# Optimization experiments

Measured on AMD Instinct MI355X. Metric: run time of the kernel, lower is better.

The kernel has to match this reference:

```python
import jax, jax.numpy as jnp
import numpy as np

VOCAB, HID, L, HEADS, INTER, MAXSEQ, NCLS = 30522, 128, 2, 2, 512, 512, 2
HEAD = HID // HEADS
B, S = 128, 512


def _tlin(x, W, b):
    # TernaryLinear: threshold-quantize W to {-1,0,1} with per-tensor scale,
    # then ordinary linear. delta = 0.7*mean|W|, alpha = mean|W| over kept entries.
    absW = jnp.abs(W)
    delta = 0.7 * jnp.mean(absW)
    mask = (absW > delta).astype(W.dtype)
    alpha = jnp.sum(absW * mask) / jnp.maximum(jnp.sum(mask), 1.0)
    Wq = jnp.sign(W) * mask * alpha  # [out, in]
    return jnp.einsum('...i,oi->...o', x, Wq) + b


def _ln(x, g, b, eps=1e-5):
    m = jnp.mean(x, axis=-1, keepdims=True)
    v = jnp.var(x, axis=-1, keepdims=True)
    return (x - m) * jax.lax.rsqrt(v + eps) * g + b


def setup_inputs() -> dict:
    key = jax.random.key(0)
    ks = iter(jax.random.split(key, 64))
    n = lambda shape, s=0.02: jax.random.normal(next(ks), shape, dtype=jnp.float32) * s
    inp = {
        'input_ids': jax.random.randint(next(ks), (B, S), 0, VOCAB, dtype=jnp.int32).astype(jnp.int64),
        'tok_emb': n((VOCAB, HID)),
        'pos_emb': n((MAXSEQ, HID)),
        'ln_g': jnp.ones((HID,), jnp.float32), 'ln_b': jnp.zeros((HID,), jnp.float32),
        'qw': n((L, HID, HID)), 'qb': jnp.zeros((L, HID), jnp.float32),
        'kw': n((L, HID, HID)), 'kb': jnp.zeros((L, HID), jnp.float32),
        'vw': n((L, HID, HID)), 'vb': jnp.zeros((L, HID), jnp.float32),
        'aow': n((L, HID, HID)), 'aob': jnp.zeros((L, HID), jnp.float32),
        'iw': n((L, INTER, HID)), 'ib': jnp.zeros((L, INTER), jnp.float32),
        'fow': n((L, HID, INTER)), 'fob': jnp.zeros((L, HID), jnp.float32),
        'ln1g': jnp.ones((L, HID), jnp.float32), 'ln1b': jnp.zeros((L, HID), jnp.float32),
        'ln2g': jnp.ones((L, HID), jnp.float32), 'ln2b': jnp.zeros((L, HID), jnp.float32),
        'clf_w': n((NCLS, HID)), 'clf_b': jnp.zeros((NCLS,), jnp.float32),
    }
    return inp


def reference(input_ids, tok_emb, pos_emb, ln_g, ln_b, qw, qb, kw, kb, vw, vb,
              aow, aob, iw, ib, fow, fob, ln1g, ln1b, ln2g, ln2b, clf_w, clf_b):
    b, s = input_ids.shape
    x = tok_emb[input_ids] + pos_emb[jnp.arange(s)][None, :, :]  # [B,S,H]
    x = _ln(x, ln_g, ln_b)
    scale = 1.0 / (HEAD ** 0.5)
    for l in range(L):
        q = _tlin(x, qw[l], qb[l]).reshape(b, s, HEADS, HEAD)
        k = _tlin(x, kw[l], kb[l]).reshape(b, s, HEADS, HEAD)
        v = _tlin(x, vw[l], vb[l]).reshape(b, s, HEADS, HEAD)
        scores = jnp.einsum('bqhd,bkhd->bhqk', q, k) * scale
        attn = jax.nn.softmax(scores, axis=-1)
        ctx = jnp.einsum('bhqk,bkhd->bqhd', attn, v).reshape(b, s, HID)
        attn_out = _tlin(ctx, aow[l], aob[l])
        x = _ln(x + attn_out, ln1g[l], ln1b[l])
        ff = _tlin(jax.nn.relu(_tlin(x, iw[l], ib[l])), fow[l], fob[l])
        x = _ln(x + ff, ln2g[l], ln2b[l])
    cls = x[:, 0, :]
    logits = _tlin(cls, clf_w, clf_b)  # [B, NCLS]
    return logits
```

## Files before the change

kernel.cpp:

```cpp
#include <hip/hip_runtime.h>

typedef short bf8s __attribute__((ext_vector_type(8)));
typedef float f32x4 __attribute__((ext_vector_type(4)));

#define MFMA16(a, b, c) __builtin_amdgcn_mfma_f32_16x16x32_bf16(a, b, c, 0, 0, 0)

constexpr int S_ = 512, HID_ = 128, B_ = 128, M_ = B_ * S_;

__device__ inline short f2bf(float f) {
  unsigned u = __float_as_uint(f);
  u = (u + 0x7fffu + ((u >> 16) & 1u)) >> 16;
  return (short)u;
}
__device__ inline float bf2f(short s) {
  return __uint_as_float(((unsigned)(unsigned short)s) << 16);
}

__device__ __forceinline__ void async16(void* lds, const void* g) {
  __builtin_amdgcn_global_load_lds(
      (const __attribute__((address_space(1))) unsigned int*)g,
      (__attribute__((address_space(3))) unsigned int*)lds, 16, 0, 0);
}

__device__ __forceinline__ bf8s ldsb(const short* base, int byteoff) {
  return *(const bf8s*)((const char*)base + byteoff);
}

__device__ inline float block_red1024(float v, float* red) {
  #pragma unroll
  for (int m = 32; m >= 1; m >>= 1) v += __shfl_xor(v, m);
  __syncthreads();
  if ((threadIdx.x & 63) == 0) red[threadIdx.x >> 6] = v;
  __syncthreads();
  float t = 0.f;
  #pragma unroll
  for (int i = 0; i < 16; ++i) t += red[i];
  return t;
}

__device__ inline void mat_info(int mat, const float* qw, const float* kw,
                                const float* vw, const float* aow, const float* iw,
                                const float* fw, const float* cw,
                                const float** src, int* n, int* doff, int* lc) {
  if (mat < 6) {
    int l = mat / 3, which = mat % 3;
    const float* t[3] = {qw, kw, vw};
    *src = t[which] + l * 16384; *n = 16384; *doff = l * 49152 + which * 16384;
    *lc = 7;
  } else if (mat < 8) {
    int l = mat - 6;
    *src = aow + l * 16384; *n = 16384; *doff = 98304 + l * 16384; *lc = 7;
  } else if (mat < 10) {
    *src = iw + (mat - 8) * 65536; *n = 65536; *doff = 131072 + (mat - 8) * 65536;
    *lc = 7;
  } else if (mat < 12) {
    *src = fw + (mat - 10) * 65536; *n = 65536; *doff = 262144 + (mat - 10) * 65536;
    *lc = 9;
  } else {
    *src = cw; *n = 256; *doff = 393216; *lc = 0;
  }
}

__global__ __launch_bounds__(1024) void k_qe(const float* qw, const float* kw,
    const float* vw, const float* aow, const float* iw, const float* fw,
    const float* cw, short* WQ,
    const int* __restrict__ ids, const float* __restrict__ tok,
    const float* __restrict__ pos, const float* __restrict__ g,
    const float* __restrict__ bb, short* xb) {
  __shared__ float red[16];
  int tid = threadIdx.x;
  if (blockIdx.x < 13) {
    const float* src; int n, doff, lc;
    mat_info(blockIdx.x, qw, kw, vw, aow, iw, fw, cw, &src, &n, &doff, &lc);
    float s = 0.f;
    for (int i = tid; i < n; i += 1024) s += fabsf(src[i]);
    s = block_red1024(s, red);
    float delta = 0.7f * s / (float)n;
    float s2 = 0.f, c2 = 0.f;
    for (int i = tid; i < n; i += 1024) {
      float a = fabsf(src[i]);
      if (a > delta) { s2 += a; c2 += 1.f; }
    }
    s2 = block_red1024(s2, red);
    c2 = block_red1024(c2, red);
    float alpha = s2 / fmaxf(c2, 1.f);
    if (lc) {
      int nf8 = n >> 3;
      for (int fo8 = tid; fo8 < nf8; fo8 += 1024) {
        int fo = fo8 << 3;
        int tile = fo >> (lc + 4);
        int rem = fo & ((16 << lc) - 1);
        int kblk = rem >> 9;
        int rem2 = rem & 511;
        int sub = rem2 >> 7;
        int r16 = (rem2 >> 3) & 15;
        int r = (tile << 4) | r16;
        int cbase = (kblk << 5) | (sub << 3);
        const float* sp = src + ((size_t)r << lc) + cbase;
        float4 w0 = *(const float4*)(sp);
        float4 w1 = *(const float4*)(sp + 4);
        float wv[8] = {w0.x, w0.y, w0.z, w0.w, w1.x, w1.y, w1.z, w1.w};
        bf8s q;
        #pragma unroll
        for (int j = 0; j < 8; ++j) {
          float w = wv[j];
          q[j] = (fabsf(w) > delta) ? f2bf(w > 0.f ? alpha : -alpha) : (short)0;
        }
        *(bf8s*)(WQ + doff + fo) = q;
      }
    } else {
      for (int i = tid; i < n; i += 1024) {
        float w = src[i];
        WQ[doff + i] = (fabsf(w) > delta) ? f2bf(w > 0.f ? alpha : -alpha) : (short)0;
      }
    }
  } else {
    int wave = tid >> 6, lane = tid & 63;
    int half = lane >> 5, l32 = lane & 31;
    int t = (blockIdx.x - 13) * 32 + wave * 2 + half;
    int s = t & (S_ - 1);
    int id = ids[t];
    int d0 = l32 * 4;
    float4 te = *(const float4*)(tok + (size_t)id * HID_ + d0);
    float4 pe = *(const float4*)(pos + (size_t)s * HID_ + d0);
    float e0 = te.x + pe.x, e1 = te.y + pe.y, e2 = te.z + pe.z, e3 = te.w + pe.w;
    float sum = e0 + e1 + e2 + e3;
    float ssq = e0 * e0 + e1 * e1 + e2 * e2 + e3 * e3;
    #pragma unroll
    for (int m = 16; m >= 1; m >>= 1) {
      sum += __shfl_xor(sum, m);
      ssq += __shfl_xor(ssq, m);
    }
    float mean = sum / 128.f;
    float var = ssq / 128.f - mean * mean;
    float rs = rsqrtf(var + 1e-5f);
    float4 g4 = *(const float4*)(g + d0);
    float4 b4 = *(const float4*)(bb + d0);
    short4 o;
    o.x = f2bf((e0 - mean) * rs * g4.x + b4.x);
    o.y = f2bf((e1 - mean) * rs * g4.y + b4.y);
    o.z = f2bf((e2 - mean) * rs * g4.z + b4.z);
    o.w = f2bf((e3 - mean) * rs * g4.w + b4.w);
    *(short4*)(xb + (size_t)t * HID_ + d0) = o;
  }
}

__global__ __launch_bounds__(256) void k_qkv(
    const short* __restrict__ A, const short* __restrict__ W,
    const float* __restrict__ b0, const float* __restrict__ b1,
    const float* __restrict__ b2, short* outb) {
  __shared__ short Wl[16384];
  int tid = threadIdx.x, lane = tid & 63, wave = tid >> 6;
  int row16 = lane & 15, quad = lane >> 4;
  int tok0 = blockIdx.x * 64 + wave * 16;

  const char* Wm = (const char*)W + blockIdx.y * 32768;
  #pragma unroll
  for (int t = 0; t < 8; ++t)
    async16((char*)Wl + t * 4096 + wave * 1024,
            Wm + t * 4096 + wave * 1024 + lane * 16);

  const short* arow = A + (size_t)(tok0 + row16) * 128 + quad * 8;
  bf8s av[4];
  #pragma unroll
  for (int ki = 0; ki < 4; ++ki) av[ki] = *(const bf8s*)(arow + ki * 32);
  __syncthreads();

  f32x4 acc[8] = {};
  #pragma unroll
  for (int ki = 0; ki < 4; ++ki)
    #pragma unroll
    for (int ot = 0; ot < 8; ++ot) {
      bf8s b = ldsb(Wl, ot * 4096 + ki * 1024 + lane * 16);
      acc[ot] = MFMA16(av[ki], b, acc[ot]);
    }

  const float* bp = (blockIdx.y == 0) ? b0 : ((blockIdx.y == 1) ? b1 : b2);
  float osc = (blockIdx.y == 0) ? 0.125f : 1.0f;
  int m0 = tok0 + quad * 4;
  #pragma unroll
  for (int ot = 0; ot < 8; ++ot) {
    int col = ot * 16 + row16;
    float bi = bp[col];
    #pragma unroll
    for (int r = 0; r < 4; ++r) {
      float v = (acc[ot][r] + bi) * osc;
      outb[(size_t)(m0 + r) * 384 + blockIdx.y * 128 + col] = f2bf(v);
    }
  }
}

template <int DOQKV>
__global__ __launch_bounds__(512, 4) void k_aoff(
    const short* __restrict__ cb, const short* __restrict__ Wa,
    const float* __restrict__ aob, const float* __restrict__ ln1g,
    const float* __restrict__ ln1b, const short* __restrict__ Wi,
    const short* __restrict__ Wf, const float* __restrict__ ib,
    const float* __restrict__ fb, const float* __restrict__ ln2g,
    const float* __restrict__ ln2b, short* xb,
    const short* __restrict__ Wqkv2, const float* __restrict__ qb2,
    const float* __restrict__ kb2, const float* __restrict__ vb2,
    short* qkvout) {
  __shared__ short SM[39936];
  int tid = threadIdx.x, lane = tid & 63, wave = tid >> 6;
  int row16 = lane & 15, quad = lane >> 4;
  int tok0 = blockIdx.x * 128 + wave * 16;
  short* mySt = SM + 16384 + wave * 640;
  short* myX  = SM + 21504 + wave * 2304;
  int xr = lane >> 2, xs = (lane & 3) * 32;
  int lb = lane * 16;

  {
    #pragma unroll
    for (int t = 0; t < 4; ++t)
      async16((char*)SM + t * 8192 + wave * 1024,
              (const char*)Wa + t * 8192 + wave * 1024 + lb);
    const short* src = xb + (size_t)(tok0 + xr) * HID_ + xs;
    bf8s x0 = *(const bf8s*)(src);
    bf8s x1 = *(const bf8s*)(src + 8);
    bf8s x2 = *(const bf8s*)(src + 16);
    bf8s x3 = *(const bf8s*)(src + 24);
    short* dst = myX + xr * 144 + xs;
    *(bf8s*)(dst) = x0;      *(bf8s*)(dst + 8) = x1;
    *(bf8s*)(dst + 16) = x2; *(bf8s*)(dst + 24) = x3;
  }

  const short* arow = cb + (size_t)(tok0 + row16) * 128 + quad * 8;
  bf8s av[4];
  #pragma unroll
  for (int ki = 0; ki < 4; ++ki) av[ki] = *(const bf8s*)(arow + ki * 32);
  __syncthreads();

  f32x4 acc[8] = {};
  #pragma unroll
  for (int ki = 0; ki < 4; ++ki)
    #pragma unroll
    for (int ot = 0; ot < 8; ++ot) {
      bf8s b = ldsb(SM, ot * 4096 + ki * 1024 + lb);
      acc[ot] = MFMA16(av[ki], b, acc[ot]);
    }
  __syncthreads();

  {
    async16((char*)SM + wave * 1024, (const char*)Wi + wave * 1024 + lb);
    async16((char*)SM + 16384 + wave * 1024,
            (const char*)Wf + wave * 16384 + lb);
  }

  {
    float sum[4] = {}, ssq[4] = {};
    #pragma unroll
    for (int ot = 0; ot < 8; ++ot) {
      int col = ot * 16 + row16;
      float bi = aob[col];
      #pragma unroll
      for (int r = 0; r < 4; ++r) {
        float v = acc[ot][r] + bi + bf2f(myX[(quad * 4 + r) * 144 + col]);
        acc[ot][r] = v;
        sum[r] += v; ssq[r] += v * v;
      }
    }
    #pragma unroll
    for (int m = 1; m <= 8; m <<= 1)
      #pragma unroll
      for (int r = 0; r < 4; ++r) {
        sum[r] += __shfl_xor(sum[r], m);
        ssq[r] += __shfl_xor(ssq[r], m);
      }
    float mean[4], rstd[4];
    #pragma unroll
    for (int r = 0; r < 4; ++r) {
      mean[r] = sum[r] / 128.f;
      float var = ssq[r] / 128.f - mean[r] * mean[r];
      rstd[r] = rsqrtf(var + 1e-5f);
    }
    #pragma unroll
    for (int ot = 0; ot < 8; ++ot) {
      int col = ot * 16 + row16;
      float gg = ln1g[col], bb2 = ln1b[col];
      #pragma unroll
      for (int r = 0; r < 4; ++r)
        acc[ot][r] = (acc[ot][r] - mean[r]) * rstd[r] * gg + bb2;
    }
  }

  #pragma unroll
  for (int ot = 0; ot < 8; ++ot) {
    int col = ot * 16 + row16;
    #pragma unroll
    for (int r = 0; r < 4; ++r)
      myX[(quad * 4 + r) * 144 + col] = f2bf(acc[ot][r]);
  }
  #pragma unroll
  for (int ki = 0; ki < 4; ++ki)
    av[ki] = *(const bf8s*)(myX + row16 * 144 + ki * 32 + quad * 8);
  __syncthreads();

  f32x4 acc2[8] = {};
  for (int c = 0; c < 16; ++c) {
    int side = c & 1;
    if (c < 15) {
      int cn = c + 1, sn = cn & 1;
      async16((char*)SM + sn * 8192 + wave * 1024,
              (const char*)Wi + cn * 8192 + wave * 1024 + lb);
      async16((char*)SM + 16384 + sn * 8192 + wave * 1024,
              (const char*)Wf + wave * 16384 + cn * 1024 + lb);
    } else if (DOQKV) {
      async16((char*)SM + wave * 1024, (const char*)Wqkv2 + wave * 1024 + lb);
      async16((char*)SM + 16384 + wave * 1024,
              (const char*)Wqkv2 + 8192 + wave * 1024 + lb);
    }

    #pragma unroll
    for (int ot = 0; ot < 2; ++ot) {
      f32x4 hacc = {};
      #pragma unroll
      for (int ki = 0; ki < 4; ++ki) {
        bf8s b = ldsb(SM, side * 8192 + ot * 4096 + ki * 1024 + lb);
        hacc = MFMA16(av[ki], b, hacc);
      }
      float bi = ib[c * 32 + ot * 16 + row16];
      #pragma unroll
      for (int r = 0; r < 4; ++r)
        mySt[(quad * 4 + r) * 40 + ot * 16 + row16] =
            f2bf(fmaxf(hacc[r] + bi, 0.f));
    }
    bf8s ha = *(const bf8s*)(mySt + row16 * 40 + quad * 8);
    #pragma unroll
    for (int ot = 0; ot < 8; ++ot) {
      bf8s bB = ldsb(SM, 16384 + side * 8192 + ot * 1024 + lb);
      acc2[ot] = MFMA16(ha, bB, acc2[ot]);
    }
    __syncthreads();
  }

  {
    float sum[4] = {}, ssq[4] = {};
    #pragma unroll
    for (int ot = 0; ot < 8; ++ot) {
      int col = ot * 16 + row16;
      float bi = fb[col];
      #pragma unroll
      for (int r = 0; r < 4; ++r) {
        float v = acc2[ot][r] + bi + bf2f(myX[(quad * 4 + r) * 144 + col]);
        acc2[ot][r] = v;
        sum[r] += v; ssq[r] += v * v;
      }
    }
    #pragma unroll
    for (int m = 1; m <= 8; m <<= 1)
      #pragma unroll
      for (int r = 0; r < 4; ++r) {
        sum[r] += __shfl_xor(sum[r], m);
        ssq[r] += __shfl_xor(ssq[r], m);
      }
    float mean[4], rstd[4];
    #pragma unroll
    for (int r = 0; r < 4; ++r) {
      mean[r] = sum[r] / 128.f;
      float var = ssq[r] / 128.f - mean[r] * mean[r];
      rstd[r] = rsqrtf(var + 1e-5f);
    }
    #pragma unroll
    for (int ot = 0; ot < 8; ++ot) {
      int col = ot * 16 + row16;
      float gg = ln2g[col], bb2 = ln2b[col];
      #pragma unroll
      for (int r = 0; r < 4; ++r)
        acc2[ot][r] = (acc2[ot][r] - mean[r]) * rstd[r] * gg + bb2;
    }
  }

  #pragma unroll
  for (int ot = 0; ot < 8; ++ot) {
    int col = ot * 16 + row16;
    #pragma unroll
    for (int r = 0; r < 4; ++r)
      myX[(quad * 4 + r) * 144 + col] = f2bf(acc2[ot][r]);
  }
  {
    const short* src = myX + xr * 144 + xs;
    short* dst = xb + (size_t)(tok0 + xr) * HID_ + xs;
    #pragma unroll
    for (int j = 0; j < 4; ++j)
      *(bf8s*)(dst + j * 8) = *(const bf8s*)(src + j * 8);
  }

  if (DOQKV) {
    bf8s av2[4];
    #pragma unroll
    for (int ki = 0; ki < 4; ++ki)
      av2[ki] = *(const bf8s*)(myX + row16 * 144 + ki * 32 + quad * 8);
    for (int j = 0; j < 6; ++j) {
      int side = j & 1;
      if (j < 5) {
        int jn = j + 1, sn = jn & 1;
        async16((char*)SM + sn * 8192 + wave * 1024,
                (const char*)Wqkv2 + jn * 16384 + wave * 1024 + lb);
        async16((char*)SM + 16384 + sn * 8192 + wave * 1024,
                (const char*)Wqkv2 + jn * 16384 + 8192 + wave * 1024 + lb);
      }
      f32x4 acc3[4] = {};
      #pragma unroll
      for (int ki = 0; ki < 4; ++ki)
        #pragma unroll
        for (int ot = 0; ot < 4; ++ot) {
          int bb_ = (ot < 2) ? side * 8192 + ot * 4096
                             : 16384 + side * 8192 + (ot - 2) * 4096;
          bf8s b = ldsb(SM, bb_ + ki * 1024 + lb);
          acc3[ot] = MFMA16(av2[ki], b, acc3[ot]);
        }
      const float* bp = (j < 2) ? qb2 : ((j < 4) ? kb2 : vb2);
      float osc = (j < 2) ? 0.125f : 1.0f;
      #pragma unroll
      for (int ot = 0; ot < 4; ++ot) {
        int col = ot * 16 + row16;
        float bi = bp[(j & 1) * 64 + col];
        #pragma unroll
        for (int r = 0; r < 4; ++r)
          myX[(quad * 4 + r) * 144 + col] = f2bf((acc3[ot][r] + bi) * osc);
      }
      {
        int xr2 = lane >> 2, xs2 = (lane & 3) * 16;
        const short* src = myX + xr2 * 144 + xs2;
        short* dst = qkvout + (size_t)(tok0 + xr2) * 384 + j * 64 + xs2;
        *(bf8s*)(dst) = *(const bf8s*)(src);
        *(bf8s*)(dst + 8) = *(const bf8s*)(src + 8);
      }
      __syncthreads();
    }
  }
}

__global__ __launch_bounds__(512) void k_attn(const short* __restrict__ qkv,
                                              short* __restrict__ O) {
  __shared__ short Kl[64 * 72];
  __shared__ short Vtl[64 * 72];
  __shared__ short Pl[8][16 * 72];

  int tid = threadIdx.x, lane = tid & 63, wave = tid >> 6;
  int row16 = lane & 15, quad = lane >> 4;
  int b = blockIdx.x >> 2, h = (blockIdx.x >> 1) & 1, qhalf = blockIdx.x & 1;
  const short* base  = qkv + (size_t)b * S_ * 384;
  const short* kbase = base + 128 + h * 64;
  const short* vbase = base + 256 + h * 64;
  int q0 = qhalf * 256 + wave * 32;

  bf8s qa[2][2];
  #pragma unroll
  for (int qf = 0; qf < 2; ++qf) {
    const short* qrow = base + h * 64 +
        (size_t)(q0 + qf * 16 + row16) * 384 + quad * 8;
    qa[qf][0] = *(const bf8s*)(qrow);
    qa[qf][1] = *(const bf8s*)(qrow + 32);
  }

  int krow = tid >> 3, dgk = tid & 7;
  int vkey = tid & 63, dgv = tid >> 6;
  const short* kptr = kbase + (size_t)krow * 384 + dgk * 8;
  const short* vptr = vbase + (size_t)vkey * 384 + dgv * 8;
  bf8s kst = *(const bf8s*)(kptr);
  bf8s vst = *(const bf8s*)(vptr);

  float li[2][4] = {};
  f32x4 oacc[2][4] = {};
  short* myP = &Pl[wave][0];

  for (int kt0 = 0; kt0 < S_; kt0 += 64) {
    if (kt0) __syncthreads();
    *(bf8s*)(&Kl[krow * 72 + dgk * 8]) = kst;
    #pragma unroll
    for (int j = 0; j < 8; ++j) Vtl[(dgv * 8 + j) * 72 + vkey] = vst[j];
    __syncthreads();
    if (kt0 + 64 < S_) {
      kst = *(const bf8s*)(kptr + (size_t)(kt0 + 64) * 384);
      vst = *(const bf8s*)(vptr + (size_t)(kt0 + 64) * 384);
    }

    f32x4 sc[2][4] = {};
    #pragma unroll
    for (int ks = 0; ks < 4; ++ks) {
      const short* kp = &Kl[(ks * 16 + row16) * 72 + quad * 8];
      bf8s k0 = *(const bf8s*)(kp);
      bf8s k1 = *(const bf8s*)(kp + 32);
      sc[0][ks] = MFMA16(qa[0][0], k0, sc[0][ks]);
      sc[0][ks] = MFMA16(qa[0][1], k1, sc[0][ks]);
      sc[1][ks] = MFMA16(qa[1][0], k0, sc[1][ks]);
      sc[1][ks] = MFMA16(qa[1][1], k1, sc[1][ks]);
    }

    #pragma unroll
    for (int qf = 0; qf < 2; ++qf) {
      #pragma unroll
      for (int ks = 0; ks < 4; ++ks)
        #pragma unroll
        for (int r = 0; r < 4; ++r) {
          float pv = __expf(sc[qf][ks][r]);
          li[qf][r] += pv;
          myP[(quad * 4 + r) * 72 + ks * 16 + row16] = f2bf(pv);
        }
      bf8s pa0 = *(const bf8s*)(&myP[row16 * 72 + quad * 8]);
      bf8s pa1 = *(const bf8s*)(&myP[row16 * 72 + 32 + quad * 8]);
      #pragma unroll
      for (int dt = 0; dt < 4; ++dt) {
        const short* vp = &Vtl[(dt * 16 + row16) * 72 + quad * 8];
        bf8s v0 = *(const bf8s*)(vp);
        bf8s v1 = *(const bf8s*)(vp + 32);
        oacc[qf][dt] = MFMA16(pa0, v0, oacc[qf][dt]);
        oacc[qf][dt] = MFMA16(pa1, v1, oacc[qf][dt]);
      }
    }
  }

  #pragma unroll
  for (int qf = 0; qf < 2; ++qf) {
    float inv[4];
    #pragma unroll
    for (int r = 0; r < 4; ++r) {
      float t = li[qf][r];
      #pragma unroll
      for (int m = 1; m <= 8; m <<= 1) t += __shfl_xor(t, m);
      inv[r] = 1.f / t;
    }
    size_t trow = (size_t)(b * S_ + q0 + qf * 16 + quad * 4);
    #pragma unroll
    for (int dt = 0; dt < 4; ++dt)
      #pragma unroll
      for (int r = 0; r < 4; ++r)
        O[(trow + r) * HID_ + h * 64 + dt * 16 + row16] =
            f2bf(oacc[qf][dt][r] * inv[r]);
  }
}

__global__ __launch_bounds__(256) void k_clf(const short* __restrict__ xb,
    const short* __restrict__ Wc, const float* __restrict__ cbias, float* out) {
  int i = threadIdx.x;
  int b = i >> 1, c = i & 1;
  float s = 0.f;
  for (int k = 0; k < HID_; ++k)
    s += bf2f(xb[(size_t)b * S_ * HID_ + k]) * bf2f(Wc[c * HID_ + k]);
  out[b * 2 + c] = s + cbias[c];
}

extern "C" void kernel_launch(void* const* d_in, const int* in_sizes, int n_in,
                              void* d_out, int out_size, void* d_ws, size_t ws_size,
                              hipStream_t stream) {
  const int*   ids     = (const int*)d_in[0];
  const float* tok_emb = (const float*)d_in[1];
  const float* pos_emb = (const float*)d_in[2];
  const float* ln_g    = (const float*)d_in[3];
  const float* ln_bb   = (const float*)d_in[4];
  const float* qw      = (const float*)d_in[5];
  const float* qbias   = (const float*)d_in[6];
  const float* kw      = (const float*)d_in[7];
  const float* kbias   = (const float*)d_in[8];
  const float* vw      = (const float*)d_in[9];
  const float* vbias   = (const float*)d_in[10];
  const float* aow     = (const float*)d_in[11];
  const float* aobias  = (const float*)d_in[12];
  const float* iw      = (const float*)d_in[13];
  const float* ibias   = (const float*)d_in[14];
  const float* fow     = (const float*)d_in[15];
  const float* fbias   = (const float*)d_in[16];
  const float* ln1g    = (const float*)d_in[17];
  const float* ln1b    = (const float*)d_in[18];
  const float* ln2g    = (const float*)d_in[19];
  const float* ln2b    = (const float*)d_in[20];
  const float* clfw    = (const float*)d_in[21];
  const float* clfb    = (const float*)d_in[22];

  char* ws = (char*)d_ws;
  short* WQ  = (short*)ws;
  short* xb  = (short*)(ws + 1048576);
  short* qkv = (short*)(ws + 1048576 + 16777216);
  short* cb_ = qkv + (size_t)M_ * 384;

  k_qe<<<13 + M_ / 32, 1024, 0, stream>>>(qw, kw, vw, aow, iw, fow, clfw, WQ,
                                          ids, tok_emb, pos_emb, ln_g, ln_bb, xb);

  const short* Wqkv0 = WQ;
  const short* Wqkv1 = WQ + 49152;
  const short* Wa0   = WQ + 98304;
  const short* Wa1   = WQ + 98304 + 16384;
  const short* Wi0   = WQ + 131072;
  const short* Wi1   = WQ + 131072 + 65536;
  const short* Wf0   = WQ + 262144;
  const short* Wf1   = WQ + 262144 + 65536;

  k_qkv<<<dim3(M_ / 64, 3), 256, 0, stream>>>(
      xb, Wqkv0, qbias, kbias, vbias, qkv);
  k_attn<<<512, 512, 0, stream>>>(qkv, cb_);
  k_aoff<1><<<M_ / 128, 512, 0, stream>>>(
      cb_, Wa0, aobias, ln1g, ln1b, Wi0, Wf0, ibias, fbias, ln2g, ln2b, xb,
      Wqkv1, qbias + HID_, kbias + HID_, vbias + HID_, qkv);
  k_attn<<<512, 512, 0, stream>>>(qkv, cb_);
  k_aoff<0><<<M_ / 128, 512, 0, stream>>>(
      cb_, Wa1, aobias + HID_, ln1g + HID_, ln1b + HID_, Wi1, Wf1,
      ibias + 512, fbias + HID_, ln2g + HID_, ln2b + HID_, xb,
      nullptr, nullptr, nullptr, nullptr, nullptr);

  k_clf<<<1, 256, 0, stream>>>(xb, WQ + 393216, clfb, (float*)d_out);
}
```

Measured before the change: 306.5 us.

## Unroll weight-stat loads, stage QKV output through LDS, parallelize classifier

Three changes. The ternary-quantization statistics loops now issue eight independent loads per thread per iteration, giving more memory-level parallelism. The QKV projection writes its bf16 results into an LDS scratch tile, reusing the weight buffer after a barrier, and then stores full 16-byte row segments instead of scattered 2-byte writes. The classifier becomes one 64-lane block per batch row with a shuffle reduction instead of a single 256-thread block doing serial dot products. The cost is an extra barrier and LDS round-trip in the QKV kernel.

```diff
diff --git a/kernel.cpp b/kernel.cpp
--- a/kernel.cpp
+++ b/kernel.cpp
@@ -73,13 +73,37 @@
     const float* src; int n, doff, lc;
     mat_info(blockIdx.x, qw, kw, vw, aow, iw, fw, cw, &src, &n, &doff, &lc);
     float s = 0.f;
-    for (int i = tid; i < n; i += 1024) s += fabsf(src[i]);
+    if (n >= 8192) {
+      for (int i0 = tid; i0 < n; i0 += 8192) {
+        float v[8];
+        #pragma unroll
+        for (int j = 0; j < 8; ++j) v[j] = src[i0 + j * 1024];
+        #pragma unroll
+        for (int j = 0; j < 8; ++j) s += fabsf(v[j]);
+      }
+    } else {
+      for (int i = tid; i < n; i += 1024) s += fabsf(src[i]);
+    }
     s = block_red1024(s, red);
     float delta = 0.7f * s / (float)n;
     float s2 = 0.f, c2 = 0.f;
-    for (int i = tid; i < n; i += 1024) {
-      float a = fabsf(src[i]);
-      if (a > delta) { s2 += a; c2 += 1.f; }
+    if (n >= 8192) {
+      for (int i0 = tid; i0 < n; i0 += 8192) {
+        float v[8];
+        #pragma unroll
+        for (int j = 0; j < 8; ++j) v[j] = src[i0 + j * 1024];
+        #pragma unroll
+        for (int j = 0; j < 8; ++j) {
+          float a = fabsf(v[j]);
+          s2 += (a > delta) ? a : 0.f;
+          c2 += (a > delta) ? 1.f : 0.f;
+        }
+      }
+    } else {
+      for (int i = tid; i < n; i += 1024) {
+        float a = fabsf(src[i]);
+        if (a > delta) { s2 += a; c2 += 1.f; }
+      }
     }
     s2 = block_red1024(s2, red);
     c2 = block_red1024(c2, red);
@@ -174,19 +198,26 @@
       bf8s b = ldsb(Wl, ot * 4096 + ki * 1024 + lane * 16);
       acc[ot] = MFMA16(av[ki], b, acc[ot]);
     }
+  __syncthreads();
 
   const float* bp = (blockIdx.y == 0) ? b0 : ((blockIdx.y == 1) ? b1 : b2);
   float osc = (blockIdx.y == 0) ? 0.125f : 1.0f;
-  int m0 = tok0 + quad * 4;
+  short* scr = Wl + wave * 2112;
   #pragma unroll
   for (int ot = 0; ot < 8; ++ot) {
     int col = ot * 16 + row16;
     float bi = bp[col];
     #pragma unroll
-    for (int r = 0; r < 4; ++r) {
-      float v = (acc[ot][r] + bi) * osc;
-      outb[(size_t)(m0 + r) * 384 + blockIdx.y * 128 + col] = f2bf(v);
-    }
+    for (int r = 0; r < 4; ++r)
+      scr[(quad * 4 + r) * 132 + col] = f2bf((acc[ot][r] + bi) * osc);
+  }
+  {
+    int rr = lane >> 2, cg = lane & 3;
+    const short* src = scr + rr * 132 + cg * 32;
+    short* dst = outb + (size_t)(tok0 + rr) * 384 + blockIdx.y * 128 + cg * 32;
+    #pragma unroll
+    for (int j = 0; j < 4; ++j)
+      *(bf8s*)(dst + j * 8) = *(const bf8s*)(src + j * 8);
   }
 }
 
@@ -532,14 +563,19 @@
   }
 }
 
-__global__ __launch_bounds__(256) void k_clf(const short* __restrict__ xb,
+__global__ __launch_bounds__(64) void k_clf(const short* __restrict__ xb,
     const short* __restrict__ Wc, const float* __restrict__ cbias, float* out) {
-  int i = threadIdx.x;
-  int b = i >> 1, c = i & 1;
-  float s = 0.f;
-  for (int k = 0; k < HID_; ++k)
-    s += bf2f(xb[(size_t)b * S_ * HID_ + k]) * bf2f(Wc[c * HID_ + k]);
-  out[b * 2 + c] = s + cbias[c];
+  int b = blockIdx.x, lane = threadIdx.x;
+  const short* xr = xb + (size_t)b * S_ * HID_;
+  float x0 = bf2f(xr[lane * 2]), x1 = bf2f(xr[lane * 2 + 1]);
+  #pragma unroll
+  for (int c = 0; c < 2; ++c) {
+    float s = x0 * bf2f(Wc[c * HID_ + lane * 2]) +
+              x1 * bf2f(Wc[c * HID_ + lane * 2 + 1]);
+    #pragma unroll
+    for (int m = 32; m >= 1; m >>= 1) s += __shfl_xor(s, m);
+    if (lane == 0) out[b * 2 + c] = s + cbias[c];
+  }
 }
 
 extern "C" void kernel_launch(void* const* d_in, const int* in_sizes, int n_in,
@@ -599,5 +635,5 @@
       ibias + 512, fbias + HID_, ln2g + HID_, ln2b + HID_, xb,
       nullptr, nullptr, nullptr, nullptr, nullptr);
 
-  k_clf<<<1, 256, 0, stream>>>(xb, WQ + 393216, clfb, (float*)d_out);
-}
+  k_clf<<<128, 64, 0, stream>>>(xb, WQ + 393216, clfb, (float*)d_out);
+}
```

After: 295.5 us. 1.04x faster.
